# Optimization experiments

Measured on AMD Instinct MI355X. Metric: run time of the kernel, lower is better.

The kernel has to match this reference:

```python
import jax, jax.numpy as jnp
import numpy as np

WH, WW = 8, 8
DIM, HEADS = 512, 16
HEAD_DIM = DIM // HEADS
SCALE = HEAD_DIM ** (-0.5)


def _rel_pos_index(wh, ww):
    # Swin relative position index, computed once with numpy (static).
    coords = np.stack(np.meshgrid(np.arange(wh), np.arange(ww), indexing='ij'))  # [2,wh,ww]
    cf = coords.reshape(2, -1)                                # [2, N]
    rel = cf[:, :, None] - cf[:, None, :]                     # [2, N, N]
    rel = rel.transpose(1, 2, 0).astype(np.int64)             # [N, N, 2]
    rel[..., 0] += wh - 1
    rel[..., 1] += ww - 1
    rel[..., 0] *= 2 * ww - 1
    return jnp.asarray(rel.sum(-1))                           # [N, N]

REL_IDX = _rel_pos_index(WH, WW)


def setup_inputs() -> dict:
    key = jax.random.key(0)
    ks = jax.random.split(key, 12)
    B_, N, C = 1024, WH * WW, DIM
    nW = 64
    std = C ** (-0.5)
    return {
        'q': jax.random.normal(ks[0], (B_, N, C), jnp.float32),
        'k': jax.random.normal(ks[1], (B_, N, C), jnp.float32),
        'v': jax.random.normal(ks[2], (B_, N, C), jnp.float32),
        'mask': jnp.zeros((nW, N, N), jnp.float32),
        'Wq': jax.random.normal(ks[3], (C, C), jnp.float32) * std,
        'bq': jnp.zeros((C,), jnp.float32),
        'Wk': jax.random.normal(ks[4], (C, C), jnp.float32) * std,
        'bk': jnp.zeros((C,), jnp.float32),
        'Wv': jax.random.normal(ks[5], (C, C), jnp.float32) * std,
        'bv': jnp.zeros((C,), jnp.float32),
        'Wp': jax.random.normal(ks[6], (C, C), jnp.float32) * std,
        'bp': jnp.zeros((C,), jnp.float32),
        'bias_table': jax.random.normal(ks[7], ((2 * WH - 1) * (2 * WW - 1), HEADS), jnp.float32) * 0.02,
    }


def reference(q, k, v, mask, Wq, bq, Wk, bk, Wv, bv, Wp, bp, bias_table):
    B_, N, C = q.shape
    H, hd = HEADS, HEAD_DIM

    def heads(x, W, b):  # Linear then split heads -> [B_, H, N, hd]
        return (x @ W.T + b).reshape(B_, N, H, hd).transpose(0, 2, 1, 3)

    qh = heads(q, Wq, bq) * SCALE
    kh = heads(k, Wk, bk)
    vh = heads(v, Wv, bv)

    attn = jnp.einsum('bhnd,bhmd->bhnm', qh, kh)              # [B_, H, N, N]
    rel_bias = bias_table[REL_IDX.reshape(-1)].reshape(N, N, H).transpose(2, 0, 1)  # [H,N,N]
    attn = attn + rel_bias[None]

    nW = mask.shape[0]
    attn = attn.reshape(B_ // nW, nW, H, N, N) + mask[None, :, None]
    attn = attn.reshape(B_, H, N, N)
    attn = jax.nn.softmax(attn, axis=-1)

    x = jnp.einsum('bhnm,bhmd->bhnd', attn, vh)
    x = x.transpose(0, 2, 1, 3).reshape(B_, N, C)
    return x @ Wp.T + bp
```

## Files before the change

### kernel.cpp

```cpp
#include <hip/hip_runtime.h>
#include <hip/hip_bf16.h>

typedef __attribute__((ext_vector_type(4))) float  f32x4;
typedef __attribute__((ext_vector_type(8))) short  bf16x8;
typedef __attribute__((ext_vector_type(4))) short  short4_t;
typedef unsigned short u16;

#define SCALE_Q 0.17677669529663687f

__device__ __forceinline__ u16 f2bf(float f) {
    union { float f; unsigned u; } v; v.f = f;
    unsigned u = v.u;
    return (u16)((u + 0x7FFFu + ((u >> 16) & 1u)) >> 16);
}

__device__ __forceinline__ void load_lds16(const void* g, void* l) {
    __builtin_amdgcn_global_load_lds(
        (const __attribute__((address_space(1))) void*)g,
        (__attribute__((address_space(3))) void*)l, 16, 0, 0);
}

__global__ __launch_bounds__(256) void cvt_kernel(
        const float* __restrict__ s, u16* __restrict__ d, int n8)
{
    const int i = blockIdx.x * 256 + threadIdx.x;
    if (i >= n8) return;
    const float4* sp = (const float4*)s + (size_t)i * 2;
    const float4 a = sp[0], b = sp[1];
    bf16x8 o;
    o[0] = (short)f2bf(a.x); o[1] = (short)f2bf(a.y);
    o[2] = (short)f2bf(a.z); o[3] = (short)f2bf(a.w);
    o[4] = (short)f2bf(b.x); o[5] = (short)f2bf(b.y);
    o[6] = (short)f2bf(b.z); o[7] = (short)f2bf(b.w);
    *((bf16x8*)d + i) = o;
}

__global__ __launch_bounds__(256) void cwb_kernel(
        const float* __restrict__ bias_table,
        const float* __restrict__ mask,
        float* __restrict__ cwb)
{
    const int wh = blockIdx.x;
    const int w = wh >> 4, h = wh & 15;
    for (int e = threadIdx.x; e < 4096; e += 256) {
        const int i = e >> 6, j = e & 63;
        const int rel = ((i >> 3) - (j >> 3) + 7) * 15 + (i & 7) - (j & 7) + 7;
        cwb[(size_t)wh * 4096 + e] = bias_table[rel * 16 + h] + mask[(size_t)w * 4096 + e];
    }
}

template<int OMODE>
__global__ __launch_bounds__(256) void gemm_bf16(
        const u16* __restrict__ A, const u16* __restrict__ Wb,
        const float* __restrict__ bias, float scale, void* __restrict__ outp)
{
    __shared__ __align__(16) u16 As[8192];
    __shared__ __align__(16) u16 Bs[8192];

    const int t  = threadIdx.x;
    const int m0 = blockIdx.y << 7;
    const int n0 = blockIdx.x << 7;
    const int lane = t & 63, wv = t >> 6;
    const int g = lane >> 4, ln = lane & 15;
    const int wr = wv >> 1, wc = wv & 1;
    const int wbase = wv << 6;

    f32x4 acc[4][4];
#pragma unroll
    for (int i = 0; i < 4; i++)
#pragma unroll
        for (int j = 0; j < 4; j++) acc[i][j] = {0.f, 0.f, 0.f, 0.f};

    const u16* Abase = A  + (size_t)m0 * 512;
    const u16* Bbase = Wb + (size_t)n0 * 512;

    for (int k0 = 0; k0 < 512; k0 += 64) {
#pragma unroll
        for (int c = 0; c < 4; c++) {
            const int bi  = (c << 8) + wbase + lane;
            const int row = bi >> 3;
            const int cbs = (bi & 7) ^ (row & 7);
            const size_t go = (size_t)row * 512 + k0 + (cbs << 3);
            u16* ldst = (c & 1) ? &Bs[(((c >> 1) << 9) + (wbase << 1)) << 3]
                                : &As[(((c >> 1) << 9) + (wbase << 1)) << 3];
            (void)ldst;
            load_lds16(Abase + go, &As[((c << 8) + wbase) << 3]);
            load_lds16(Bbase + go, &Bs[((c << 8) + wbase) << 3]);
        }
        __syncthreads();
#pragma unroll
        for (int ks = 0; ks < 2; ks++) {
            bf16x8 af[4], bfr[4];
#pragma unroll
            for (int mt = 0; mt < 4; mt++) {
                const int row = (wr << 6) + (mt << 4) + ln;
                af[mt] = *(const bf16x8*)&As[(row << 6) + ((((ks << 2) + g) ^ (row & 7)) << 3)];
            }
#pragma unroll
            for (int nt = 0; nt < 4; nt++) {
                const int row = (wc << 6) + (nt << 4) + ln;
                bfr[nt] = *(const bf16x8*)&Bs[(row << 6) + ((((ks << 2) + g) ^ (row & 7)) << 3)];
            }
#pragma unroll
            for (int mt = 0; mt < 4; mt++)
#pragma unroll
                for (int nt = 0; nt < 4; nt++)
                    acc[mt][nt] = __builtin_amdgcn_mfma_f32_16x16x32_bf16(
                        af[mt], bfr[nt], acc[mt][nt], 0, 0, 0);
        }
        __syncthreads();
    }

#pragma unroll
    for (int mt = 0; mt < 4; mt++) {
#pragma unroll
        for (int nt = 0; nt < 4; nt++) {
            const int n = n0 + (wc << 6) + (nt << 4) + ln;
            const float bv = bias[n];
            const int mbase = m0 + (wr << 6) + (mt << 4) + (g << 2);
            if (OMODE == 0) {
#pragma unroll
                for (int r = 0; r < 4; r++) {
                    const int m = mbase + r;
                    const int b = m >> 6, tt = m & 63, hh = n >> 5, d = n & 31;
                    ((u16*)outp)[((size_t)(b * 16 + hh) * 64 + tt) * 32 + d] =
                        f2bf((acc[mt][nt][r] + bv) * scale);
                }
            } else if (OMODE == 1) {
                short4_t hq;
#pragma unroll
                for (int r = 0; r < 4; r++) hq[r] = (short)f2bf((acc[mt][nt][r] + bv) * scale);
                const int b = mbase >> 6, tt = mbase & 63, hh = n >> 5, d = n & 31;
                *(short4_t*)&((u16*)outp)[((size_t)(b * 16 + hh) * 32 + d) * 64 + tt] = hq;
            } else {
#pragma unroll
                for (int r = 0; r < 4; r++) {
                    const int m = mbase + r;
                    ((float*)outp)[(size_t)m * 512 + n] = (acc[mt][nt][r] + bv) * scale;
                }
            }
        }
    }
}

__global__ __launch_bounds__(64) void attn_kernel(
        const u16* __restrict__ qh, const u16* __restrict__ kh,
        const u16* __restrict__ vt, const float* __restrict__ cwb,
        u16* __restrict__ xout)
{
    __shared__ __align__(16) u16 P[4096];

    const int bid = blockIdx.x;
    const int b = bid >> 4, h = bid & 15, w = b & 63;
    const int lane = threadIdx.x, g = lane >> 4, ln = lane & 15;
    const size_t base = (size_t)bid * 2048;

    bf16x8 kf[4], qf[4];
#pragma unroll
    for (int mt = 0; mt < 4; mt++)
        kf[mt] = *(const bf16x8*)&kh[base + (mt * 16 + ln) * 32 + g * 8];
#pragma unroll
    for (int nt = 0; nt < 4; nt++)
        qf[nt] = *(const bf16x8*)&qh[base + (nt * 16 + ln) * 32 + g * 8];

    f32x4 acc[4][4];
#pragma unroll
    for (int i = 0; i < 4; i++)
#pragma unroll
        for (int j = 0; j < 4; j++) acc[i][j] = {0.f, 0.f, 0.f, 0.f};

#pragma unroll
    for (int mt = 0; mt < 4; mt++)
#pragma unroll
        for (int nt = 0; nt < 4; nt++)
            acc[mt][nt] = __builtin_amdgcn_mfma_f32_16x16x32_bf16(
                kf[mt], qf[nt], acc[mt][nt], 0, 0, 0);

    const float* cw = cwb + (size_t)(w * 16 + h) * 4096;
#pragma unroll
    for (int nt = 0; nt < 4; nt++) {
        const int i = nt * 16 + ln;
#pragma unroll
        for (int mt = 0; mt < 4; mt++) {
            const float4 bm = *(const float4*)&cw[i * 64 + mt * 16 + (g << 2)];
            acc[mt][nt][0] += bm.x; acc[mt][nt][1] += bm.y;
            acc[mt][nt][2] += bm.z; acc[mt][nt][3] += bm.w;
        }
    }

#pragma unroll
    for (int nt = 0; nt < 4; nt++) {
        float mx = acc[0][nt][0];
#pragma unroll
        for (int mt = 0; mt < 4; mt++)
#pragma unroll
            for (int r = 0; r < 4; r++) mx = fmaxf(mx, acc[mt][nt][r]);
        mx = fmaxf(mx, __shfl_xor(mx, 16));
        mx = fmaxf(mx, __shfl_xor(mx, 32));
        float sum = 0.f;
#pragma unroll
        for (int mt = 0; mt < 4; mt++)
#pragma unroll
            for (int r = 0; r < 4; r++) {
                const float p = __expf(acc[mt][nt][r] - mx);
                acc[mt][nt][r] = p;
                sum += p;
            }
        sum += __shfl_xor(sum, 16);
        sum += __shfl_xor(sum, 32);
        const float rs = 1.0f / sum;
        const int i = nt * 16 + ln;
#pragma unroll
        for (int mt = 0; mt < 4; mt++) {
            short4_t hq;
#pragma unroll
            for (int r = 0; r < 4; r++) hq[r] = (short)f2bf(acc[mt][nt][r] * rs);
            const int idx = (i * 64 + mt * 16 + (g << 2)) ^ ((i & 7) << 3);
            *(short4_t*)&P[idx] = hq;
        }
    }
    __syncthreads();

    f32x4 oacc[2][4];
#pragma unroll
    for (int i = 0; i < 2; i++)
#pragma unroll
        for (int j = 0; j < 4; j++) oacc[i][j] = {0.f, 0.f, 0.f, 0.f};

#pragma unroll
    for (int ks = 0; ks < 2; ks++) {
        bf16x8 vf[2], pf[4];
#pragma unroll
        for (int mt = 0; mt < 2; mt++)
            vf[mt] = *(const bf16x8*)&vt[base + (mt * 16 + ln) * 64 + ks * 32 + g * 8];
#pragma unroll
        for (int nt = 0; nt < 4; nt++) {
            const int i = nt * 16 + ln;
            pf[nt] = *(const bf16x8*)&P[(i * 64 + ks * 32 + g * 8) ^ ((i & 7) << 3)];
        }
#pragma unroll
        for (int mt = 0; mt < 2; mt++)
#pragma unroll
            for (int nt = 0; nt < 4; nt++)
                oacc[mt][nt] = __builtin_amdgcn_mfma_f32_16x16x32_bf16(
                    vf[mt], pf[nt], oacc[mt][nt], 0, 0, 0);
    }

#pragma unroll
    for (int mt = 0; mt < 2; mt++) {
#pragma unroll
        for (int nt = 0; nt < 4; nt++) {
            const int i = nt * 16 + ln, d0 = mt * 16 + (g << 2);
            short4_t hq;
#pragma unroll
            for (int r = 0; r < 4; r++) hq[r] = (short)f2bf(oacc[mt][nt][r]);
            *(short4_t*)&xout[((size_t)b * 64 + i) * 512 + h * 32 + d0] = hq;
        }
    }
}

extern "C" void kernel_launch(void* const* d_in, const int* in_sizes, int n_in,
                              void* d_out, int out_size, void* d_ws, size_t ws_size,
                              hipStream_t stream) {
    const float* q    = (const float*)d_in[0];
    const float* k    = (const float*)d_in[1];
    const float* v    = (const float*)d_in[2];
    const float* mask = (const float*)d_in[3];
    const float* Wq   = (const float*)d_in[4];
    const float* bq   = (const float*)d_in[5];
    const float* Wk   = (const float*)d_in[6];
    const float* bk   = (const float*)d_in[7];
    const float* Wv   = (const float*)d_in[8];
    const float* bv   = (const float*)d_in[9];
    const float* Wp   = (const float*)d_in[10];
    const float* bp   = (const float*)d_in[11];
    const float* bias_table = (const float*)d_in[12];
    float* out = (float*)d_out;

    char* ws = (char*)d_ws;
    u16*   t0  = (u16*)(ws);
    u16*   qh  = (u16*)(ws + 67108864);
    u16*   kh  = (u16*)(ws + 134217728);
    u16*   vt  = (u16*)(ws + 201326592);
    float* cwb = (float*)(ws + 268435456);
    u16*   wqb = (u16*)(ws + 285212672);
    u16*   wkb = (u16*)(ws + 285736960);
    u16*   wvb = (u16*)(ws + 286261248);
    u16*   wpb = (u16*)(ws + 286785536);

    const int n8_act = (1024 * 64 * 512) / 8;
    const int n8_w   = (512 * 512) / 8;

    cwb_kernel<<<1024, 256, 0, stream>>>(bias_table, mask, cwb);
    cvt_kernel<<<n8_w / 256, 256, 0, stream>>>(Wq, wqb, n8_w);
    cvt_kernel<<<n8_w / 256, 256, 0, stream>>>(Wk, wkb, n8_w);
    cvt_kernel<<<n8_w / 256, 256, 0, stream>>>(Wv, wvb, n8_w);
    cvt_kernel<<<n8_w / 256, 256, 0, stream>>>(Wp, wpb, n8_w);

    cvt_kernel<<<n8_act / 256, 256, 0, stream>>>(q, t0, n8_act);
    gemm_bf16<0><<<dim3(4, 512), 256, 0, stream>>>(t0, wqb, bq, SCALE_Q, (void*)qh);

    cvt_kernel<<<n8_act / 256, 256, 0, stream>>>(k, t0, n8_act);
    gemm_bf16<0><<<dim3(4, 512), 256, 0, stream>>>(t0, wkb, bk, 1.0f, (void*)kh);

    cvt_kernel<<<n8_act / 256, 256, 0, stream>>>(v, t0, n8_act);
    gemm_bf16<1><<<dim3(4, 512), 256, 0, stream>>>(t0, wvb, bv, 1.0f, (void*)vt);

    attn_kernel<<<16384, 64, 0, stream>>>(qh, kh, vt, cwb, t0);

    gemm_bf16<2><<<dim3(4, 512), 256, 0, stream>>>(t0, wpb, bp, 1.0f, (void*)out);
}
```

Before: 459.2 us.

## Fuse fp32-to-bf16 activation conversion into GEMM loads and batch attention heads

The Q/K/V projection GEMMs now load fp32 activations directly into LDS and convert to bf16 while building MFMA fragments. This removes the three separate full-tensor conversion kernels and their round-trip through workspace. Blocks are remapped with an XCD-aware swizzle, and the attention kernel packs four head-windows per 256-thread block. Manual bf16 rounding is replaced with the native __bf16 cast. The cost is doubled LDS for the A tile and extra per-fragment conversion work inside the GEMM inner loop.

Result: faster. 417.7 us (-9.0%).

```diff
diff --git a/kernel.cpp b/kernel.cpp
--- a/kernel.cpp
+++ b/kernel.cpp
@@ -8,10 +8,16 @@
 
 #define SCALE_Q 0.17677669529663687f
 
-__device__ __forceinline__ u16 f2bf(float f) {
-    union { float f; unsigned u; } v; v.f = f;
-    unsigned u = v.u;
-    return (u16)((u + 0x7FFFu + ((u >> 16) & 1u)) >> 16);
+__device__ __forceinline__ short bfc(float f) {
+    __bf16 b = (__bf16)f;
+    union { __bf16 b; short s; } u; u.b = b; return u.s;
+}
+
+__device__ __forceinline__ bf16x8 pack8(f32x4 a, f32x4 b) {
+    bf16x8 o;
+    o[0] = bfc(a[0]); o[1] = bfc(a[1]); o[2] = bfc(a[2]); o[3] = bfc(a[3]);
+    o[4] = bfc(b[0]); o[5] = bfc(b[1]); o[6] = bfc(b[2]); o[7] = bfc(b[3]);
+    return o;
 }
 
 __device__ __forceinline__ void load_lds16(const void* g, void* l) {
@@ -28,10 +34,8 @@
     const float4* sp = (const float4*)s + (size_t)i * 2;
     const float4 a = sp[0], b = sp[1];
     bf16x8 o;
-    o[0] = (short)f2bf(a.x); o[1] = (short)f2bf(a.y);
-    o[2] = (short)f2bf(a.z); o[3] = (short)f2bf(a.w);
-    o[4] = (short)f2bf(b.x); o[5] = (short)f2bf(b.y);
-    o[6] = (short)f2bf(b.z); o[7] = (short)f2bf(b.w);
+    o[0] = bfc(a.x); o[1] = bfc(a.y); o[2] = bfc(a.z); o[3] = bfc(a.w);
+    o[4] = bfc(b.x); o[5] = bfc(b.y); o[6] = bfc(b.z); o[7] = bfc(b.w);
     *((bf16x8*)d + i) = o;
 }
 
@@ -49,21 +53,22 @@
     }
 }
 
-template<int OMODE>
-__global__ __launch_bounds__(256) void gemm_bf16(
-        const u16* __restrict__ A, const u16* __restrict__ Wb,
+template<int AFP32, int OMODE>
+__global__ __launch_bounds__(256) void gemm_k(
+        const void* __restrict__ Aptr, const u16* __restrict__ Wb,
         const float* __restrict__ bias, float scale, void* __restrict__ outp)
 {
-    __shared__ __align__(16) u16 As[8192];
+    __shared__ __align__(16) unsigned char Asb[AFP32 ? 32768 : 16384];
     __shared__ __align__(16) u16 Bs[8192];
 
-    const int t  = threadIdx.x;
-    const int m0 = blockIdx.y << 7;
-    const int n0 = blockIdx.x << 7;
+    const int wg = (blockIdx.x & 7) * 256 + (blockIdx.x >> 3);
+    const int m0 = (wg >> 2) << 7;
+    const int n0 = (wg & 3) << 7;
+
+    const int t = threadIdx.x;
     const int lane = t & 63, wv = t >> 6;
     const int g = lane >> 4, ln = lane & 15;
     const int wr = wv >> 1, wc = wv & 1;
-    const int wbase = wv << 6;
 
     f32x4 acc[4][4];
 #pragma unroll
@@ -71,30 +76,55 @@
 #pragma unroll
         for (int j = 0; j < 4; j++) acc[i][j] = {0.f, 0.f, 0.f, 0.f};
 
-    const u16* Abase = A  + (size_t)m0 * 512;
-    const u16* Bbase = Wb + (size_t)n0 * 512;
-
     for (int k0 = 0; k0 < 512; k0 += 64) {
-#pragma unroll
-        for (int c = 0; c < 4; c++) {
-            const int bi  = (c << 8) + wbase + lane;
-            const int row = bi >> 3;
-            const int cbs = (bi & 7) ^ (row & 7);
-            const size_t go = (size_t)row * 512 + k0 + (cbs << 3);
-            u16* ldst = (c & 1) ? &Bs[(((c >> 1) << 9) + (wbase << 1)) << 3]
-                                : &As[(((c >> 1) << 9) + (wbase << 1)) << 3];
-            (void)ldst;
-            load_lds16(Abase + go, &As[((c << 8) + wbase) << 3]);
-            load_lds16(Bbase + go, &Bs[((c << 8) + wbase) << 3]);
+        if (AFP32) {
+            const float* Ab = (const float*)Aptr + (size_t)m0 * 512;
+#pragma unroll
+            for (int c = 0; c < 8; c++) {
+                const int bi  = (c << 8) + (wv << 6) + lane;
+                const int row = bi >> 4;
+                const int col = ((bi & 15) ^ (row & 7)) << 2;
+                load_lds16(Ab + (size_t)row * 512 + k0 + col,
+                           &Asb[((c << 8) + (wv << 6)) << 4]);
+            }
+        } else {
+            const u16* Ab = (const u16*)Aptr + (size_t)m0 * 512;
+#pragma unroll
+            for (int c = 0; c < 4; c++) {
+                const int bi  = (c << 8) + (wv << 6) + lane;
+                const int row = bi >> 3;
+                const int col = ((bi & 7) ^ (row & 7)) << 3;
+                load_lds16(Ab + (size_t)row * 512 + k0 + col,
+                           &Asb[((c << 8) + (wv << 6)) << 4]);
+            }
+        }
+        {
+            const u16* Bb = Wb + (size_t)n0 * 512;
+#pragma unroll
+            for (int c = 0; c < 4; c++) {
+                const int bi  = (c << 8) + (wv << 6) + lane;
+                const int row = bi >> 3;
+                const int col = ((bi & 7) ^ (row & 7)) << 3;
+                load_lds16(Bb + (size_t)row * 512 + k0 + col,
+                           &Bs[((c << 8) + (wv << 6)) << 3]);
+            }
         }
         __syncthreads();
+
 #pragma unroll
         for (int ks = 0; ks < 2; ks++) {
             bf16x8 af[4], bfr[4];
 #pragma unroll
             for (int mt = 0; mt < 4; mt++) {
                 const int row = (wr << 6) + (mt << 4) + ln;
-                af[mt] = *(const bf16x8*)&As[(row << 6) + ((((ks << 2) + g) ^ (row & 7)) << 3)];
+                if (AFP32) {
+                    const int lb = (ks << 3) + (g << 1);
+                    const f32x4 lo = *(const f32x4*)&Asb[row * 256 + (((lb    ) ^ (row & 7)) << 4)];
+                    const f32x4 hi = *(const f32x4*)&Asb[row * 256 + (((lb + 1) ^ (row & 7)) << 4)];
+                    af[mt] = pack8(lo, hi);
+                } else {
+                    af[mt] = *(const bf16x8*)&Asb[(row << 7) + ((((ks << 2) + g) ^ (row & 7)) << 4)];
+                }
             }
 #pragma unroll
             for (int nt = 0; nt < 4; nt++) {
@@ -124,12 +154,12 @@
                     const int m = mbase + r;
                     const int b = m >> 6, tt = m & 63, hh = n >> 5, d = n & 31;
                     ((u16*)outp)[((size_t)(b * 16 + hh) * 64 + tt) * 32 + d] =
-                        f2bf((acc[mt][nt][r] + bv) * scale);
+                        (u16)bfc((acc[mt][nt][r] + bv) * scale);
                 }
             } else if (OMODE == 1) {
                 short4_t hq;
 #pragma unroll
-                for (int r = 0; r < 4; r++) hq[r] = (short)f2bf((acc[mt][nt][r] + bv) * scale);
+                for (int r = 0; r < 4; r++) hq[r] = bfc((acc[mt][nt][r] + bv) * scale);
                 const int b = mbase >> 6, tt = mbase & 63, hh = n >> 5, d = n & 31;
                 *(short4_t*)&((u16*)outp)[((size_t)(b * 16 + hh) * 32 + d) * 64 + tt] = hq;
             } else {
@@ -143,17 +173,19 @@
     }
 }
 
-__global__ __launch_bounds__(64) void attn_kernel(
+__global__ __launch_bounds__(256) void attn_kernel(
         const u16* __restrict__ qh, const u16* __restrict__ kh,
         const u16* __restrict__ vt, const float* __restrict__ cwb,
         u16* __restrict__ xout)
 {
-    __shared__ __align__(16) u16 P[4096];
-
-    const int bid = blockIdx.x;
+    __shared__ __align__(16) u16 P[16384];
+
+    const int wv = threadIdx.x >> 6;
+    const int bid = (blockIdx.x << 2) + wv;
     const int b = bid >> 4, h = bid & 15, w = b & 63;
-    const int lane = threadIdx.x, g = lane >> 4, ln = lane & 15;
+    const int lane = threadIdx.x & 63, g = lane >> 4, ln = lane & 15;
     const size_t base = (size_t)bid * 2048;
+    u16* Pw = &P[wv << 12];
 
     bf16x8 kf[4], qf[4];
 #pragma unroll
@@ -214,9 +246,9 @@
         for (int mt = 0; mt < 4; mt++) {
             short4_t hq;
 #pragma unroll
-            for (int r = 0; r < 4; r++) hq[r] = (short)f2bf(acc[mt][nt][r] * rs);
+            for (int r = 0; r < 4; r++) hq[r] = bfc(acc[mt][nt][r] * rs);
             const int idx = (i * 64 + mt * 16 + (g << 2)) ^ ((i & 7) << 3);
-            *(short4_t*)&P[idx] = hq;
+            *(short4_t*)&Pw[idx] = hq;
         }
     }
     __syncthreads();
@@ -236,7 +268,7 @@
 #pragma unroll
         for (int nt = 0; nt < 4; nt++) {
             const int i = nt * 16 + ln;
-            pf[nt] = *(const bf16x8*)&P[(i * 64 + ks * 32 + g * 8) ^ ((i & 7) << 3)];
+            pf[nt] = *(const bf16x8*)&Pw[(i * 64 + ks * 32 + g * 8) ^ ((i & 7) << 3)];
         }
 #pragma unroll
         for (int mt = 0; mt < 2; mt++)
@@ -253,7 +285,7 @@
             const int i = nt * 16 + ln, d0 = mt * 16 + (g << 2);
             short4_t hq;
 #pragma unroll
-            for (int r = 0; r < 4; r++) hq[r] = (short)f2bf(oacc[mt][nt][r]);
+            for (int r = 0; r < 4; r++) hq[r] = bfc(oacc[mt][nt][r]);
             *(short4_t*)&xout[((size_t)b * 64 + i) * 512 + h * 32 + d0] = hq;
         }
     }
@@ -288,8 +320,7 @@
     u16*   wvb = (u16*)(ws + 286261248);
     u16*   wpb = (u16*)(ws + 286785536);
 
-    const int n8_act = (1024 * 64 * 512) / 8;
-    const int n8_w   = (512 * 512) / 8;
+    const int n8_w = (512 * 512) / 8;
 
     cwb_kernel<<<1024, 256, 0, stream>>>(bias_table, mask, cwb);
     cvt_kernel<<<n8_w / 256, 256, 0, stream>>>(Wq, wqb, n8_w);
@@ -297,16 +328,11 @@
     cvt_kernel<<<n8_w / 256, 256, 0, stream>>>(Wv, wvb, n8_w);
     cvt_kernel<<<n8_w / 256, 256, 0, stream>>>(Wp, wpb, n8_w);
 
-    cvt_kernel<<<n8_act / 256, 256, 0, stream>>>(q, t0, n8_act);
-    gemm_bf16<0><<<dim3(4, 512), 256, 0, stream>>>(t0, wqb, bq, SCALE_Q, (void*)qh);
-
-    cvt_kernel<<<n8_act / 256, 256, 0, stream>>>(k, t0, n8_act);
-    gemm_bf16<0><<<dim3(4, 512), 256, 0, stream>>>(t0, wkb, bk, 1.0f, (void*)kh);
-
-    cvt_kernel<<<n8_act / 256, 256, 0, stream>>>(v, t0, n8_act);
-    gemm_bf16<1><<<dim3(4, 512), 256, 0, stream>>>(t0, wvb, bv, 1.0f, (void*)vt);
-
-    attn_kernel<<<16384, 64, 0, stream>>>(qh, kh, vt, cwb, t0);
-
-    gemm_bf16<2><<<dim3(4, 512), 256, 0, stream>>>(t0, wpb, bp, 1.0f, (void*)out);
-}
+    gemm_k<1, 0><<<2048, 256, 0, stream>>>((const void*)q, wqb, bq, SCALE_Q, (void*)qh);
+    gemm_k<1, 0><<<2048, 256, 0, stream>>>((const void*)k, wkb, bk, 1.0f,    (void*)kh);
+    gemm_k<1, 1><<<2048, 256, 0, stream>>>((const void*)v, wvb, bv, 1.0f,    (void*)vt);
+
+    attn_kernel<<<4096, 256, 0, stream>>>(qh, kh, vt, cwb, t0);
+
+    gemm_k<0, 2><<<2048, 256, 0, stream>>>((const void*)t0, wpb, bp, 1.0f, (void*)out);
+}
```
